# Kernel tuning notes

Hardware: AMD Instinct MI355X
Metric: run time of the kernel (lower is better)

The kernel has to match this reference:

```python
import jax, jax.numpy as jnp
import numpy as np

B, T, A, P = 128, 128, 16, 4
D, H, Q, QI, V = 256, 512, 128, 512, 64
NUM_TRICKS = 13
SIGNAL_PHASE = 1
# static phase routing: contiguous blocks of T/P positions per phase (phase_mask buffer)
PHASE_ID = (np.arange(T) * P // T).astype(np.int32)
_DECAY = 0.6
_nt_left = NUM_TRICKS - np.arange(NUM_TRICKS, dtype=np.float32)
P_SIGNAL = ((1.0 - _DECAY) / (1.0 - _DECAY ** _nt_left)).astype(np.float32)


def setup_inputs() -> dict:
    key = jax.random.key(0)
    ks = jax.random.split(key, 12)
    a = jax.random.randint(ks[0], (B, T, A, 3), 0, V, dtype=jnp.int32)
    pad = (jax.random.uniform(ks[1], (B, T, A)) < 0.3) & (jnp.arange(A) >= 1)
    valid_actions = jnp.where(pad[..., None], -1, a)
    phase = jnp.broadcast_to(jnp.asarray(PHASE_ID), (B, T)).astype(jnp.int32)
    trick = jax.random.randint(ks[2], (B, T), 0, NUM_TRICKS, dtype=jnp.int32)
    backbone_embed = jax.random.normal(ks[3], (B, T, QI), jnp.float32)
    s = lambda k, shape, fan: jax.random.normal(k, shape, jnp.float32) / np.float32(np.sqrt(fan))
    return dict(
        backbone_embed=backbone_embed, valid_actions=valid_actions, phase=phase, trick=trick,
        emb0=s(ks[4], (V, D), D), emb1=s(ks[5], (V, D), D), emb2=s(ks[6], (V, D), D),
        ln_g=jnp.ones((D,), jnp.float32), ln_b=jnp.zeros((D,), jnp.float32),
        kW1=s(ks[7], (P, D, H), D), kb1=jnp.zeros((P, H), jnp.float32),
        kW2=s(ks[8], (P, H, H), H), kb2=jnp.zeros((P, H), jnp.float32),
        kW3=s(ks[9], (P, H, Q), H), kb3=jnp.zeros((P, Q), jnp.float32),
        qW=s(ks[10], (P, QI, Q), QI), qb=jnp.zeros((P, Q), jnp.float32),
    )


def _forward(backbone_embed, valid_actions, phase, trick,
             emb0, emb1, emb2, ln_g, ln_b,
             kW1, kb1, kW2, kb2, kW3, kb3, qW, qb):
    pid = PHASE_ID  # static (T,) routing -> gather per-position phase params (same math as mask gather/scatter)
    idx = jnp.clip(valid_actions, 0, V - 1)
    x = emb0[idx[..., 0]] + emb1[idx[..., 1]] + emb2[idx[..., 2]]  # (B,T,A,D) action embed
    mu = jnp.mean(x, -1, keepdims=True)
    var = jnp.var(x, -1, keepdims=True)
    x = (x - mu) * jax.lax.rsqrt(var + 1e-5) * ln_g + ln_b  # key LayerNorm
    # phase-branched key MLP (BranchedFF over MLP)
    h = jax.nn.relu(jnp.einsum('btad,tdh->btah', x, kW1[pid]) + kb1[pid][None, :, None, :])
    h = jax.nn.relu(jnp.einsum('btah,thg->btag', h, kW2[pid]) + kb2[pid][None, :, None, :])
    keyv = jnp.einsum('btah,thq->btaq', h, kW3[pid]) + kb3[pid][None, :, None, :]  # (B,T,A,Q)
    # phase-branched query Linear (BranchedFF over Linear)
    query = jnp.einsum('btd,tdq->btq', backbone_embed, qW[pid]) + qb[pid][None]  # (B,T,Q)
    attn = jnp.einsum('btq,btaq->bta', query, keyv) / np.float32(np.sqrt(Q))
    invalid = valid_actions[..., 0] == -1
    attn = jnp.where(invalid, -jnp.inf, attn)
    # no-signal log-weight
    n_valid = jnp.sum(~invalid, -1).astype(attn.dtype)  # (B,T)
    p_s = jnp.asarray(P_SIGNAL)[trick]
    wgt = jnp.log(jnp.maximum((1.0 - p_s) / p_s * (n_valid - 1.0), 1e-5))
    wgt = jnp.where(n_valid == 1.0, 0.0, wgt)
    attn = attn.at[..., 0].add(jnp.where(phase == SIGNAL_PHASE, wgt, 0.0))
    return jax.nn.log_softmax(attn, axis=-1)


def reference(backbone_embed, valid_actions, phase, trick,
              emb0, emb1, emb2, ln_g, ln_b,
              kW1, kb1, kW2, kb2, kW3, kb3, qW, qb):
    return _forward(backbone_embed, valid_actions, phase, trick,
                    emb0, emb1, emb2, ln_g, ln_b,
                    kW1, kb1, kW2, kb2, kW3, kb3, qW, qb)
```

## Files before the change

### kernel.cpp

```cpp
#include <hip/hip_runtime.h>
#include <hip/hip_bf16.h>
#include <cmath>

constexpr int Bc = 128, Tc = 128, Ac = 16;
constexpr int Dc = 256, Hc = 512, Qc = 128, QIc = 512, Vc = 64, NTk = 13;
constexpr float NEG_BIG = -1e30f;
constexpr float ACT_SCALE = 16.f;
constexpr float ACC_SCALE = 1.f / 256.f;

typedef unsigned int uint;
typedef uint uint2v __attribute__((ext_vector_type(2)));
typedef float f32x4 __attribute__((ext_vector_type(4)));

#define MFMA16F8(a, b, c) __builtin_amdgcn_mfma_f32_16x16x32_fp8_fp8(a, b, c, 0, 0, 0)

__device__ __forceinline__ long long u2ll(uint2v v) {
  union { uint2v u; long long l; } x;
  x.u = v;
  return x.l;
}
__device__ __forceinline__ short f2bf(float f) {
  __hip_bfloat16 h = __float2bfloat16(f);
  return *(short*)&h;
}
__device__ __forceinline__ float bf2f(short s) {
  return __uint_as_float(((unsigned)(unsigned short)s) << 16);
}
__device__ __forceinline__ uint pack4_fp8(float a, float b, float c, float d) {
  uint v = 0;
  v = __builtin_amdgcn_cvt_pk_fp8_f32(a, b, v, 0);
  v = __builtin_amdgcn_cvt_pk_fp8_f32(c, d, v, 1);
  return v;
}
__device__ __forceinline__ char f2fp8(float a) {
  return (char)(__builtin_amdgcn_cvt_pk_fp8_f32(a, a, 0, 0) & 0xFF);
}

__global__ void transform_all(const float* __restrict__ kW1, const float* __restrict__ kW2,
                              const float* __restrict__ kW3, const float* __restrict__ qW,
                              uint2v* __restrict__ kW1f, uint2v* __restrict__ kW2f,
                              uint2v* __restrict__ kW3f, uint2v* __restrict__ qWf) {
  int gid = blockIdx.x * 256 + threadIdx.x;
  const float* W;
  uint2v* dst;
  int NT, KC, N, local;
  if (gid < 65536) {
    W = kW1; dst = kW1f; NT = 32; KC = 8; N = 512; local = gid;
  } else if (gid < 196608) {
    W = kW2; dst = kW2f; NT = 32; KC = 16; N = 512; local = gid - 65536;
  } else if (gid < 229376) {
    W = kW3; dst = kW3f; NT = 8; KC = 16; N = 128; local = gid - 196608;
  } else {
    W = qW; dst = qWf; NT = 8; KC = 16; N = 128; local = gid - 229376;
  }
  int lane = local & 63;
  int frag = local >> 6;
  int kc = frag % KC;
  int rest = frag / KC;
  int nt = rest % NT;
  int p = rest / NT;
  int K = KC * 32;
  int n = nt * 16 + (lane & 15);
  int k0 = kc * 32 + (lane >> 4) * 8;
  const float* src = W + ((size_t)p * K + k0) * N + n;
  float f[8];
#pragma unroll
  for (int j = 0; j < 8; ++j) f[j] = src[(size_t)j * N] * ACT_SCALE;
  uint2v v;
  v.x = pack4_fp8(f[0], f[1], f[2], f[3]);
  v.y = pack4_fp8(f[4], f[5], f[6], f[7]);
  dst[local] = v;
}

template <int KC, int NNT, int NMT, bool RELU, int OUTMODE, int SIN, int SOUT>
__device__ __forceinline__ void layer16(
    const char* __restrict__ aB, void* __restrict__ o0,
    const uint2v* __restrict__ Wf, const float* __restrict__ bias,
    int nt0, int lane) {
  const int c = lane & 15, q = lane >> 4;
  const char* ap = aB + c * SIN + q * 8;
  const uint2v* wbase = Wf + (size_t)nt0 * KC * 64 + lane;

  f32x4 acc[NNT][NMT];
#pragma unroll
  for (int nt = 0; nt < NNT; ++nt)
#pragma unroll
    for (int mt = 0; mt < NMT; ++mt)
#pragma unroll
      for (int r = 0; r < 4; ++r) acc[nt][mt][r] = 0.f;

#pragma unroll 1
  for (int kc = 0; kc < KC; ++kc) {
    uint2v af[NMT];
#pragma unroll
    for (int mt = 0; mt < NMT; ++mt)
      af[mt] = *(const uint2v*)(ap + mt * 16 * SIN + kc * 32);
#pragma unroll
    for (int nt = 0; nt < NNT; ++nt) {
      uint2v bfv = wbase[(nt * KC + kc) * 64];
      long long bb = u2ll(bfv);
#pragma unroll
      for (int mt = 0; mt < NMT; ++mt)
        acc[nt][mt] = MFMA16F8(u2ll(af[mt]), bb, acc[nt][mt]);
    }
  }

#pragma unroll
  for (int nt = 0; nt < NNT; ++nt) {
    const int n = (nt0 + nt) * 16 + c;
    const float bn = bias[n];
#pragma unroll
    for (int mt = 0; mt < NMT; ++mt)
#pragma unroll
      for (int r = 0; r < 4; ++r) {
        int row = mt * 16 + q * 4 + r;
        float v = acc[nt][mt][r] * ACC_SCALE + bn;
        if (RELU) v = fmaxf(v, 0.f);
        if (OUTMODE == 0) {
          ((char*)o0)[row * SOUT + n] = f2fp8(v * ACT_SCALE);
        } else if (OUTMODE == 1) {
          ((short*)o0)[row * SOUT + n] = f2bf(v);
        } else {
          if (q == 0) ((float*)o0)[r * SOUT + n] = v;
        }
      }
  }
}

constexpr int SX = 264;
constexpr int SH = 520;
constexpr int SKV = 136;
constexpr int SQY = 132;

__global__ __launch_bounds__(1024, 8) void policy_main(
    const float* __restrict__ be, const int* __restrict__ va,
    const int* __restrict__ phase, const int* __restrict__ trick,
    const float* __restrict__ emb0, const float* __restrict__ emb1,
    const float* __restrict__ emb2, const float* __restrict__ ln_g,
    const float* __restrict__ ln_b,
    const float* __restrict__ kb1, const float* __restrict__ kb2,
    const float* __restrict__ kb3, const float* __restrict__ qb,
    const uint2v* __restrict__ kW1f, const uint2v* __restrict__ kW2f,
    const uint2v* __restrict__ kW3f, const uint2v* __restrict__ qWf,
    float* __restrict__ out) {
  __shared__ __align__(16) char bufA[64 * SH];
  __shared__ __align__(16) char bufB[64 * SH];
  __shared__ __align__(16) float QYs[4 * SQY];
  __shared__ float attn_s[64];
  __shared__ int inval_s[64];
  __shared__ int ph_s[4], tr_s[4];
  __shared__ int idx3_s[64][3];

  char* Xs = bufA;
  char* H2 = bufA;
  char* H1 = bufB;
  char* beA = bufB;
  short* KV = (short*)(bufB + 8320);

  const int tid = threadIdx.x;
  const int w = tid >> 6, lane = tid & 63;
  const int p = blockIdx.x & 3;
  const int g = blockIdx.x >> 2;
  const int b = g >> 3;
  const int t0 = p * 32 + (g & 7) * 4;
  const int bt0 = b * Tc + t0;

  if (tid < 64) {
    const int* vp = va + ((size_t)bt0 * Ac + tid) * 3;
    int a0 = vp[0], a1 = vp[1], a2 = vp[2];
    inval_s[tid] = (a0 == -1);
    idx3_s[tid][0] = min(max(a0, 0), Vc - 1);
    idx3_s[tid][1] = min(max(a1, 0), Vc - 1);
    idx3_s[tid][2] = min(max(a2, 0), Vc - 1);
  } else if (tid < 68) {
    ph_s[tid - 64] = phase[bt0 + tid - 64];
  } else if (tid < 72) {
    tr_s[tid - 68] = trick[bt0 + tid - 68];
  }
  __syncthreads();

  {
    const int r = tid >> 4, part = tid & 15, d0 = part * 16;
    const float4* e0 = (const float4*)(emb0 + idx3_s[r][0] * Dc + d0);
    const float4* e1 = (const float4*)(emb1 + idx3_s[r][1] * Dc + d0);
    const float4* e2 = (const float4*)(emb2 + idx3_s[r][2] * Dc + d0);
    float xv[16];
    float sum = 0.f, ss = 0.f;
#pragma unroll
    for (int j = 0; j < 4; ++j) {
      float4 v0 = e0[j], v1 = e1[j], v2 = e2[j];
      float4 v;
      v.x = v0.x + v1.x + v2.x; v.y = v0.y + v1.y + v2.y;
      v.z = v0.z + v1.z + v2.z; v.w = v0.w + v1.w + v2.w;
      xv[j * 4 + 0] = v.x; xv[j * 4 + 1] = v.y; xv[j * 4 + 2] = v.z; xv[j * 4 + 3] = v.w;
      sum += v.x + v.y + v.z + v.w;
      ss += v.x * v.x + v.y * v.y + v.z * v.z + v.w * v.w;
    }
    sum += __shfl_xor(sum, 1); sum += __shfl_xor(sum, 2);
    sum += __shfl_xor(sum, 4); sum += __shfl_xor(sum, 8);
    ss += __shfl_xor(ss, 1);   ss += __shfl_xor(ss, 2);
    ss += __shfl_xor(ss, 4);   ss += __shfl_xor(ss, 8);
    const float mu = sum / (float)Dc;
    const float rstd = rsqrtf(ss / (float)Dc - mu * mu + 1e-5f);
    float y[16];
#pragma unroll
    for (int j = 0; j < 16; ++j) {
      int d = d0 + j;
      y[j] = ((xv[j] - mu) * rstd * ln_g[d] + ln_b[d]) * ACT_SCALE;
    }
    uint2v v8;
    v8.x = pack4_fp8(y[0], y[1], y[2], y[3]);
    v8.y = pack4_fp8(y[4], y[5], y[6], y[7]);
    *(uint2v*)(Xs + r * SX + d0) = v8;
    v8.x = pack4_fp8(y[8], y[9], y[10], y[11]);
    v8.y = pack4_fp8(y[12], y[13], y[14], y[15]);
    *(uint2v*)(Xs + r * SX + d0 + 8) = v8;
  }
  __syncthreads();

  layer16<8, 2, 4, true, 0, SX, SH>(Xs, H1, kW1f + (size_t)p * 32 * 8 * 64,
                                    kb1 + p * Hc, w * 2, lane);
  __syncthreads();

  layer16<16, 2, 4, true, 0, SH, SH>(H1, H2, kW2f + (size_t)p * 32 * 16 * 64,
                                     kb2 + p * Hc, w * 2, lane);
  __syncthreads();

  if (tid < 256) {
    int tok = tid >> 6, d0 = (tid & 63) * 8;
    const float* bp = be + ((size_t)bt0 + tok) * QIc + d0;
    uint2v v8;
    v8.x = pack4_fp8(bp[0] * ACT_SCALE, bp[1] * ACT_SCALE, bp[2] * ACT_SCALE, bp[3] * ACT_SCALE);
    v8.y = pack4_fp8(bp[4] * ACT_SCALE, bp[5] * ACT_SCALE, bp[6] * ACT_SCALE, bp[7] * ACT_SCALE);
    *(uint2v*)(beA + tok * SH + d0) = v8;
  }
  __syncthreads();

  if (w < 8) {
    layer16<16, 1, 4, false, 1, SH, SKV>(H2, KV, kW3f + (size_t)p * 8 * 16 * 64,
                                         kb3 + p * Qc, w, lane);
  } else {
    layer16<16, 1, 1, false, 2, SH, SQY>(beA, QYs, qWf + (size_t)p * 8 * 16 * 64,
                                         qb + p * Qc, w - 8, lane);
  }
  __syncthreads();

  {
    const int r = tid >> 4, part = tid & 15, tok = r >> 4;
    const short* kp = KV + r * SKV + part * 8;
    const float* qp = QYs + tok * SQY + part * 8;
    float s = 0.f;
#pragma unroll
    for (int j = 0; j < 8; ++j) s += bf2f(kp[j]) * qp[j];
    s += __shfl_xor(s, 1); s += __shfl_xor(s, 2);
    s += __shfl_xor(s, 4); s += __shfl_xor(s, 8);
    if (part == 0) attn_s[r] = s * 0.08838834764831845f;
  }
  __syncthreads();

  if (tid < 4) {
    const int tok = tid;
    const int bt = bt0 + tok;
    float av[Ac];
    int nv = 0;
#pragma unroll
    for (int a = 0; a < Ac; ++a) {
      int iv = inval_s[tok * Ac + a];
      nv += iv ? 0 : 1;
      av[a] = iv ? NEG_BIG : attn_s[tok * Ac + a];
    }
    if (ph_s[tok] == 1) {
      const int nt = NTk - tr_s[tok];
      float dp = 1.f;
      for (int i = 0; i < nt; ++i) dp *= 0.6f;
      const float ps = 0.4f / (1.f - dp);
      float wgt = (nv == 1) ? 0.f : logf(fmaxf((1.f - ps) / ps * ((float)nv - 1.f), 1e-5f));
      av[0] += wgt;
    }
    float m = NEG_BIG;
#pragma unroll
    for (int a = 0; a < Ac; ++a) m = fmaxf(m, av[a]);
    float s = 0.f;
#pragma unroll
    for (int a = 0; a < Ac; ++a) s += expf(av[a] - m);
    const float lse = logf(s) + m;
#pragma unroll
    for (int a = 0; a < Ac; ++a)
      out[bt * Ac + a] = inval_s[tok * Ac + a] ? NEG_BIG : (av[a] - lse);
  }
}

extern "C" void kernel_launch(void* const* d_in, const int* in_sizes, int n_in,
                              void* d_out, int out_size, void* d_ws, size_t ws_size,
                              hipStream_t stream) {
  const float* be   = (const float*)d_in[0];
  const int*   va   = (const int*)d_in[1];
  const int*   ph   = (const int*)d_in[2];
  const int*   tr   = (const int*)d_in[3];
  const float* emb0 = (const float*)d_in[4];
  const float* emb1 = (const float*)d_in[5];
  const float* emb2 = (const float*)d_in[6];
  const float* lng  = (const float*)d_in[7];
  const float* lnb  = (const float*)d_in[8];
  const float* kW1  = (const float*)d_in[9];
  const float* kb1  = (const float*)d_in[10];
  const float* kW2  = (const float*)d_in[11];
  const float* kb2  = (const float*)d_in[12];
  const float* kW3  = (const float*)d_in[13];
  const float* kb3  = (const float*)d_in[14];
  const float* qW   = (const float*)d_in[15];
  const float* qb   = (const float*)d_in[16];
  float* out = (float*)d_out;

  uint2v* kW1f = (uint2v*)d_ws;
  uint2v* kW2f = kW1f + 65536;
  uint2v* kW3f = kW2f + 131072;
  uint2v* qWf  = kW3f + 32768;

  transform_all<<<262144 / 256, 256, 0, stream>>>(kW1, kW2, kW3, qW, kW1f, kW2f, kW3f, qWf);

  policy_main<<<4096, 1024, 0, stream>>>(be, va, ph, tr, emb0, emb1, emb2, lng, lnb,
                                         kb1, kb2, kb3, qb, kW1f, kW2f, kW3f, qWf, out);
}
```

Baseline: 350.0 us.

## Hoist backbone load into prologue, drop syncs, pad LDS strides

Moves the backbone-embedding fp8 conversion into the kernel prologue, writing it to its own shared buffer so it no longer waits behind layer 2. This removes one barrier and the idx3 staging barrier, since each thread now reads its action indices directly. LDS row strides are widened to change the bank-conflict pattern, and the epilogue folds the scale and bias into a single fma. The cost is extra shared memory, which can lower occupancy, and redundant index loads issued by 16 threads per row.

New measurement: 345.0 us. No clear change (-1.4%).

```diff
diff --git a/kernel.cpp b/kernel.cpp
--- a/kernel.cpp
+++ b/kernel.cpp
@@ -7,6 +7,7 @@
 constexpr float NEG_BIG = -1e30f;
 constexpr float ACT_SCALE = 16.f;
 constexpr float ACC_SCALE = 1.f / 256.f;
+constexpr float ACC_TO_ACT = 1.f / 16.f;
 
 typedef unsigned int uint;
 typedef uint uint2v __attribute__((ext_vector_type(2)));
@@ -79,7 +80,6 @@
     int nt0, int lane) {
   const int c = lane & 15, q = lane >> 4;
   const char* ap = aB + c * SIN + q * 8;
-  const uint2v* wbase = Wf + (size_t)nt0 * KC * 64 + lane;
 
   f32x4 acc[NNT][NMT];
 #pragma unroll
@@ -97,7 +97,8 @@
       af[mt] = *(const uint2v*)(ap + mt * 16 * SIN + kc * 32);
 #pragma unroll
     for (int nt = 0; nt < NNT; ++nt) {
-      uint2v bfv = wbase[(nt * KC + kc) * 64];
+      const uint2v* wk = Wf + ((size_t)(nt0 + nt) * KC + kc) * 64;
+      uint2v bfv = wk[lane];
       long long bb = u2ll(bfv);
 #pragma unroll
       for (int mt = 0; mt < NMT; ++mt)
@@ -109,26 +110,29 @@
   for (int nt = 0; nt < NNT; ++nt) {
     const int n = (nt0 + nt) * 16 + c;
     const float bn = bias[n];
+    const float bn16 = bn * ACT_SCALE;
 #pragma unroll
     for (int mt = 0; mt < NMT; ++mt)
 #pragma unroll
       for (int r = 0; r < 4; ++r) {
         int row = mt * 16 + q * 4 + r;
-        float v = acc[nt][mt][r] * ACC_SCALE + bn;
-        if (RELU) v = fmaxf(v, 0.f);
         if (OUTMODE == 0) {
-          ((char*)o0)[row * SOUT + n] = f2fp8(v * ACT_SCALE);
+          float v = fmaf(acc[nt][mt][r], ACC_TO_ACT, bn16);
+          if (RELU) v = fmaxf(v, 0.f);
+          ((char*)o0)[row * SOUT + n] = f2fp8(v);
         } else if (OUTMODE == 1) {
+          float v = fmaf(acc[nt][mt][r], ACC_SCALE, bn);
           ((short*)o0)[row * SOUT + n] = f2bf(v);
         } else {
+          float v = fmaf(acc[nt][mt][r], ACC_SCALE, bn);
           if (q == 0) ((float*)o0)[r * SOUT + n] = v;
         }
       }
   }
 }
 
-constexpr int SX = 264;
-constexpr int SH = 520;
+constexpr int SX = 280;
+constexpr int SH = 536;
 constexpr int SKV = 136;
 constexpr int SQY = 132;
 
@@ -145,17 +149,16 @@
     float* __restrict__ out) {
   __shared__ __align__(16) char bufA[64 * SH];
   __shared__ __align__(16) char bufB[64 * SH];
+  __shared__ __align__(16) char beAb[16 * SH];
   __shared__ __align__(16) float QYs[4 * SQY];
   __shared__ float attn_s[64];
   __shared__ int inval_s[64];
   __shared__ int ph_s[4], tr_s[4];
-  __shared__ int idx3_s[64][3];
 
   char* Xs = bufA;
   char* H2 = bufA;
   char* H1 = bufB;
-  char* beA = bufB;
-  short* KV = (short*)(bufB + 8320);
+  short* KV = (short*)bufB;
 
   const int tid = threadIdx.x;
   const int w = tid >> 6, lane = tid & 63;
@@ -166,24 +169,29 @@
   const int bt0 = b * Tc + t0;
 
   if (tid < 64) {
-    const int* vp = va + ((size_t)bt0 * Ac + tid) * 3;
-    int a0 = vp[0], a1 = vp[1], a2 = vp[2];
-    inval_s[tid] = (a0 == -1);
-    idx3_s[tid][0] = min(max(a0, 0), Vc - 1);
-    idx3_s[tid][1] = min(max(a1, 0), Vc - 1);
-    idx3_s[tid][2] = min(max(a2, 0), Vc - 1);
+    inval_s[tid] = (va[((size_t)bt0 * Ac + tid) * 3] == -1);
   } else if (tid < 68) {
     ph_s[tid - 64] = phase[bt0 + tid - 64];
   } else if (tid < 72) {
     tr_s[tid - 68] = trick[bt0 + tid - 68];
   }
-  __syncthreads();
-
+  if (tid < 256) {
+    int tok = tid >> 6, d0 = (tid & 63) * 8;
+    const float* bp = be + ((size_t)bt0 + tok) * QIc + d0;
+    uint2v v8;
+    v8.x = pack4_fp8(bp[0] * ACT_SCALE, bp[1] * ACT_SCALE, bp[2] * ACT_SCALE, bp[3] * ACT_SCALE);
+    v8.y = pack4_fp8(bp[4] * ACT_SCALE, bp[5] * ACT_SCALE, bp[6] * ACT_SCALE, bp[7] * ACT_SCALE);
+    *(uint2v*)(beAb + tok * SH + d0) = v8;
+  }
   {
     const int r = tid >> 4, part = tid & 15, d0 = part * 16;
-    const float4* e0 = (const float4*)(emb0 + idx3_s[r][0] * Dc + d0);
-    const float4* e1 = (const float4*)(emb1 + idx3_s[r][1] * Dc + d0);
-    const float4* e2 = (const float4*)(emb2 + idx3_s[r][2] * Dc + d0);
+    const int* vp = va + ((size_t)bt0 * Ac + r) * 3;
+    int i0 = min(max(vp[0], 0), Vc - 1);
+    int i1 = min(max(vp[1], 0), Vc - 1);
+    int i2 = min(max(vp[2], 0), Vc - 1);
+    const float4* e0 = (const float4*)(emb0 + i0 * Dc + d0);
+    const float4* e1 = (const float4*)(emb1 + i1 * Dc + d0);
+    const float4* e2 = (const float4*)(emb2 + i2 * Dc + d0);
     float xv[16];
     float sum = 0.f, ss = 0.f;
 #pragma unroll
@@ -226,21 +234,11 @@
                                      kb2 + p * Hc, w * 2, lane);
   __syncthreads();
 
-  if (tid < 256) {
-    int tok = tid >> 6, d0 = (tid & 63) * 8;
-    const float* bp = be + ((size_t)bt0 + tok) * QIc + d0;
-    uint2v v8;
-    v8.x = pack4_fp8(bp[0] * ACT_SCALE, bp[1] * ACT_SCALE, bp[2] * ACT_SCALE, bp[3] * ACT_SCALE);
-    v8.y = pack4_fp8(bp[4] * ACT_SCALE, bp[5] * ACT_SCALE, bp[6] * ACT_SCALE, bp[7] * ACT_SCALE);
-    *(uint2v*)(beA + tok * SH + d0) = v8;
-  }
-  __syncthreads();
-
   if (w < 8) {
     layer16<16, 1, 4, false, 1, SH, SKV>(H2, KV, kW3f + (size_t)p * 8 * 16 * 64,
                                          kb3 + p * Qc, w, lane);
   } else {
-    layer16<16, 1, 1, false, 2, SH, SQY>(beA, QYs, qWf + (size_t)p * 8 * 16 * 64,
+    layer16<16, 1, 1, false, 2, SH, SQY>(beAb, QYs, qWf + (size_t)p * 8 * 16 * 64,
                                          qb + p * Qc, w - 8, lane);
   }
   __syncthreads();
```
